# Performance work log

Measured on AMD Instinct MI355X. Metric: run time of the kernel, lower is better.

Reference implementation:

```python
import jax, jax.numpy as jnp
import numpy as np

BATCH = 1
SEQ = 3072
HID = 1024
HEADS = 16
HDIM = HID // HEADS  # 64
NSEQ = 8
SLEN = 380
ROPE_BASE = 10.0


def _boundaries():
    b, start = [], 0
    for _ in range(NSEQ):
        b.append((start, start + SLEN))
        start = start + SLEN + 1  # +1 for SEP token
    return b


def setup_inputs() -> dict:
    key = jax.random.key(0)
    ks = jax.random.split(key, 10)
    bnd = _boundaries()
    L = bnd[-1][1]  # actual_length = 3047
    # block-diagonal mask; SEP tokens attend only to themselves
    mask = np.zeros((L, L), dtype=bool)
    for s, e in bnd:
        mask[s:e, s:e] = True
    for s, e in bnd[:-1]:
        mask[e, e] = True
    # position ids reset at each sequence start
    pos = np.zeros((SEQ,), dtype=np.int32)
    for s, e in bnd:
        pos[s:e] = np.arange(e - s, dtype=np.int32)
    sc = 1.0 / np.sqrt(HID)
    return {
        "x": jax.random.normal(ks[0], (BATCH, SEQ, HID), jnp.float32),
        "wq": jax.random.normal(ks[1], (HID, HID), jnp.float32) * sc,
        "bq": jnp.zeros((HID,), jnp.float32),
        "wk": jax.random.normal(ks[2], (HID, HID), jnp.float32) * sc,
        "bk": jnp.zeros((HID,), jnp.float32),
        "wv": jax.random.normal(ks[3], (HID, HID), jnp.float32) * sc,
        "bv": jnp.zeros((HID,), jnp.float32),
        "wo": jax.random.normal(ks[4], (HID, HID), jnp.float32) * sc,
        "bo": jnp.zeros((HID,), jnp.float32),
        "mask": jnp.asarray(mask),
        "position_ids": jnp.asarray(pos)[None, :],  # [1, SEQ]
    }


def _apply_rope(q, k, pos):
    # q, k: [B, S, H, D]; pos: [B, S]
    half = HDIM // 2
    inv_freq = 1.0 / (ROPE_BASE ** (jnp.arange(0, HDIM, 2, dtype=jnp.float32) / HDIM))
    ang = pos.astype(jnp.float32)[..., None] * inv_freq  # [B, S, half]
    cos = jnp.cos(ang)[:, :, None, :]  # [B, S, 1, half]
    sin = jnp.sin(ang)[:, :, None, :]

    def rot(t):
        t1, t2 = t[..., :half], t[..., half:]
        return jnp.concatenate([t1 * cos - t2 * sin, t1 * sin + t2 * cos], axis=-1)

    return rot(q), rot(k)


def reference(x, wq, bq, wk, bk, wv, bv, wo, bo, mask, position_ids):
    B, S, _ = x.shape
    L = mask.shape[0]  # actual_length (static)
    q = (x @ wq.T + bq).reshape(B, S, HEADS, HDIM)
    k = (x @ wk.T + bk).reshape(B, S, HEADS, HDIM)
    v = (x @ wv.T + bv).reshape(B, S, HEADS, HDIM)
    q, k = _apply_rope(q, k, position_ids)
    # [B, H, S, D], trim to packed length
    q = q.transpose(0, 2, 1, 3)[:, :, :L, :]
    k = k.transpose(0, 2, 1, 3)[:, :, :L, :]
    v = v.transpose(0, 2, 1, 3)[:, :, :L, :]
    scores = jnp.einsum("bhqd,bhkd->bhqk", q, k) / jnp.sqrt(jnp.float32(HDIM))
    scores = jnp.where(mask[None, None], scores, -jnp.inf)
    attn = jax.nn.softmax(scores, axis=-1)
    out = jnp.einsum("bhqk,bhkd->bhqd", attn, v)  # [B, H, L, D]
    out = jnp.pad(out, ((0, 0), (0, 0), (0, S - L), (0, 0)))  # zero padded tail
    out = out.transpose(0, 2, 1, 3).reshape(B, S, HID)
    return out @ wo.T + bo
```

## Files before the change

kernel.cpp:

```cpp
#include <hip/hip_runtime.h>

typedef unsigned short u16;
typedef __attribute__((ext_vector_type(8))) short short8;
typedef __attribute__((ext_vector_type(4))) float f32x4;

#define SEQ 3072
#define HID 1024
#define HEADS 16
#define HDIM 64
#define SEGLEN 380
#define SEGSTR 381
#define NSEG 8
#define LTOT 3047
#define VPAD 384

static __device__ __forceinline__ u16 f2bf(float f) {
  unsigned u = __builtin_bit_cast(unsigned, f);
  u += 0x7fffu + ((u >> 16) & 1u);
  return (u16)(u >> 16);
}
static __device__ __forceinline__ float bf2f(u16 h) {
  unsigned u = ((unsigned)h) << 16;
  return __builtin_bit_cast(float, u);
}

static __device__ __forceinline__ void load_lds16(const void* g, void* l) {
  __builtin_amdgcn_global_load_lds((const __attribute__((address_space(1))) void*)g,
                                   (__attribute__((address_space(3))) void*)l, 16, 0, 0);
}

#define BAR() __builtin_amdgcn_s_barrier()
#define VM(N) asm volatile("s_waitcnt vmcnt(" #N ")" ::: "memory")

__global__ void cvt_all_kernel(const float* __restrict__ x, const float* __restrict__ wq,
                               const float* __restrict__ wk, const float* __restrict__ wv,
                               const float* __restrict__ wo, u16* __restrict__ ws) {
  const int d = blockIdx.x * 256 + threadIdx.x;
  const float* src;
  if (d < 393216) {
    const int tm = d >> 14, rem = d & 16383;
    const int tk = rem >> 9, rem2 = rem & 511;
    const int row = rem2 >> 2, cp = rem2 & 3;
    const int j = cp ^ ((row >> 1) & 3);
    src = x + ((size_t)(tm * 128 + row) * HID + tk * 32 + j * 8);
  } else if (d < 786432) {
    const int dd = d - 393216;
    const int tc = dd >> 14, rem = dd & 16383;
    const int tk = rem >> 9, rem2 = rem & 511;
    const int row = rem2 >> 2, cp = rem2 & 3;
    const int j = cp ^ ((row >> 1) & 3);
    const int which = tc >> 3;
    const float* wsrc = (which == 0) ? wq : (which == 1) ? wk : wv;
    src = wsrc + ((size_t)((tc & 7) * 128 + row) * HID + tk * 32 + j * 8);
  } else {
    const int dd = d - 786432;
    const int tc = dd >> 13, rem = dd & 8191;
    const int tk = rem >> 9, rem2 = rem & 511;
    const int row = rem2 >> 3, cp = rem2 & 7;
    const int j = cp ^ (row & 7);
    src = wo + ((size_t)(tc * 64 + row) * HID + tk * 64 + j * 8);
  }
  float4 a = *reinterpret_cast<const float4*>(src);
  float4 b = *reinterpret_cast<const float4*>(src + 4);
  unsigned long long o0 = (unsigned long long)f2bf(a.x) |
                          ((unsigned long long)f2bf(a.y) << 16) |
                          ((unsigned long long)f2bf(a.z) << 32) |
                          ((unsigned long long)f2bf(a.w) << 48);
  unsigned long long o1 = (unsigned long long)f2bf(b.x) |
                          ((unsigned long long)f2bf(b.y) << 16) |
                          ((unsigned long long)f2bf(b.z) << 32) |
                          ((unsigned long long)f2bf(b.w) << 48);
  unsigned long long* dst = reinterpret_cast<unsigned long long*>(ws + (size_t)d * 8);
  dst[0] = o0;
  dst[1] = o1;
}

static __device__ __forceinline__ void stage_qkv(
    const u16* __restrict__ Ablk, const u16* __restrict__ Bblk,
    u16* As, u16* Bs, int t) {
  const int tid = threadIdx.x;
  const int w = tid >> 6;
  load_lds16(Ablk + (size_t)t * 4096 + tid * 8, As + (w * 64) * 8);
  load_lds16(Bblk + (size_t)t * 4096 + tid * 8, Bs + (w * 64) * 8);
}

static __device__ __forceinline__ void compute_qkv(
    const u16* As, const u16* Bs, int wr, int cb0, int lc, int lh, f32x4 (*acc)[2]) {
  short8 af[4], bfv[2];
#pragma unroll
  for (int m = 0; m < 4; ++m) {
    const int row = wr + m * 16 + lc;
    af[m] = *reinterpret_cast<const short8*>(As + row * 32 + (lh ^ ((row >> 1) & 3)) * 8);
  }
#pragma unroll
  for (int n = 0; n < 2; ++n) {
    const int row = cb0 + n * 32 + lc;
    bfv[n] = *reinterpret_cast<const short8*>(Bs + row * 32 + (lh ^ ((row >> 1) & 3)) * 8);
  }
  __builtin_amdgcn_s_setprio(1);
#pragma unroll
  for (int m = 0; m < 4; ++m)
#pragma unroll
    for (int n = 0; n < 2; ++n)
      acc[m][n] = __builtin_amdgcn_mfma_f32_16x16x32_bf16(af[m], bfv[n], acc[m][n], 0, 0, 0);
  __builtin_amdgcn_s_setprio(0);
}

__global__ __launch_bounds__(512) void qkv_gemm_kernel(
    const u16* __restrict__ xblk, const u16* __restrict__ wblk,
    const float* __restrict__ bq, const float* __restrict__ bk, const float* __restrict__ bv,
    u16* __restrict__ qb, u16* __restrict__ kbuf, u16* __restrict__ vT) {
  __shared__ u16 As[3][128 * 32];
  __shared__ u16 Bs[3][128 * 32];
  const int which = blockIdx.y >> 3;
  const float* bias = (which == 0) ? bq : (which == 1) ? bk : bv;
  const int rowBase = blockIdx.x * 128;
  const int colBase = (blockIdx.y & 7) * 128;
  const u16* Ablk = xblk + (size_t)blockIdx.x * 131072;
  const u16* Bblk = wblk + (size_t)blockIdx.y * 131072;
  const int tid = threadIdx.x;
  const int w = tid >> 6, l = tid & 63, lc = l & 15, lh = l >> 4;
  const int wr = (w >> 2) * 64;
  const int c2 = w & 3;
  const int cb0 = (c2 >> 1) * 64 + (c2 & 1) * 16;

  f32x4 acc[4][2];
  f32x4 z4 = {0.f, 0.f, 0.f, 0.f};
#pragma unroll
  for (int m = 0; m < 4; ++m) { acc[m][0] = z4; acc[m][1] = z4; }

  stage_qkv(Ablk, Bblk, As[0], Bs[0], 0);
  stage_qkv(Ablk, Bblk, As[1], Bs[1], 1);
#pragma unroll 1
  for (int t = 0; t < 30; t += 3) {
    stage_qkv(Ablk, Bblk, As[2], Bs[2], t + 2);
    VM(4); BAR();
    compute_qkv(As[0], Bs[0], wr, cb0, lc, lh, acc);
    BAR();
    stage_qkv(Ablk, Bblk, As[0], Bs[0], t + 3);
    VM(4); BAR();
    compute_qkv(As[1], Bs[1], wr, cb0, lc, lh, acc);
    BAR();
    stage_qkv(Ablk, Bblk, As[1], Bs[1], t + 4);
    VM(4); BAR();
    compute_qkv(As[2], Bs[2], wr, cb0, lc, lh, acc);
    BAR();
  }
  VM(2); BAR();
  compute_qkv(As[0], Bs[0], wr, cb0, lc, lh, acc);
  BAR();
  VM(0); BAR();
  compute_qkv(As[1], Bs[1], wr, cb0, lc, lh, acc);

  const int f = (c2 & 1) * 16 + lc;
  const int col0 = colBase + (c2 >> 1) * 64 + f;
  if (which < 2) {
    u16* outp = which ? kbuf : qb;
    const float bv0 = bias[col0];
    const float bv1 = bias[col0 + 32];
    const float invf = exp2f(-(float)f * 0.10381025296523007f);
#pragma unroll
    for (int m = 0; m < 4; ++m) {
      const int row0 = rowBase + wr + m * 16 + lh * 4;
#pragma unroll
      for (int r = 0; r < 4; ++r) {
        const int row = row0 + r;
        const int rr = row % SEGSTR;
        const float pos = (float)((rr < SEGLEN) ? rr : 0);
        float sn, cs;
        sincosf(pos * invf, &sn, &cs);
        const float t1 = acc[m][0][r] + bv0;
        const float t2 = acc[m][1][r] + bv1;
        const size_t base = (size_t)row * HID + col0;
        outp[base] = f2bf(t1 * cs - t2 * sn);
        outp[base + 32] = f2bf(t1 * sn + t2 * cs);
      }
    }
  } else {
#pragma unroll
    for (int n = 0; n < 2; ++n) {
      const int col = col0 + n * 32;
      const float bvl = bias[col];
#pragma unroll
      for (int m = 0; m < 4; ++m) {
        const int row0 = rowBase + wr + m * 16 + lh * 4;
#pragma unroll
        for (int r = 0; r < 4; ++r) {
          const float v = acc[m][n][r] + bvl;
          const int row = row0 + r;
          const int sg = row / SEGSTR;
          const int j = row - sg * SEGSTR;
          if (sg < NSEG)
            vT[(size_t)col * (NSEG * VPAD) + sg * VPAD + j] = f2bf(v);
        }
      }
    }
  }
}

static __device__ __forceinline__ void stage_out(
    const u16* __restrict__ Ab, const u16* __restrict__ Bb,
    u16* As, u16* Bs, int t) {
  const int tid = threadIdx.x;
  const int w = tid >> 6;
#pragma unroll
  for (int c = 0; c < 2; ++c)
    load_lds16(Ab + (size_t)t * 8192 + (c * 512 + tid) * 8, As + (c * 512 + w * 64) * 8);
  load_lds16(Bb + (size_t)t * 4096 + tid * 8, Bs + (w * 64) * 8);
}

static __device__ __forceinline__ void compute_out(
    const u16* As, const u16* Bs, int wrO, int wcO, int lc, int lh, f32x4 (*acc)[2]) {
  short8 af[2][2], bfv[2][2];
#pragma unroll
  for (int m = 0; m < 2; ++m) {
    const int row = wrO + m * 16 + lc;
#pragma unroll
    for (int ks = 0; ks < 2; ++ks)
      af[m][ks] = *reinterpret_cast<const short8*>(
          As + row * 64 + (((ks * 4 + lh) ^ (row & 7))) * 8);
  }
#pragma unroll
  for (int n = 0; n < 2; ++n) {
    const int row = wcO + n * 16 + lc;
#pragma unroll
    for (int ks = 0; ks < 2; ++ks)
      bfv[n][ks] = *reinterpret_cast<const short8*>(
          Bs + row * 64 + (((ks * 4 + lh) ^ (row & 7))) * 8);
  }
  __builtin_amdgcn_s_setprio(1);
#pragma unroll
  for (int ks = 0; ks < 2; ++ks)
#pragma unroll
    for (int m = 0; m < 2; ++m)
#pragma unroll
      for (int n = 0; n < 2; ++n)
        acc[m][n] = __builtin_amdgcn_mfma_f32_16x16x32_bf16(af[m][ks], bfv[n][ks], acc[m][n], 0, 0, 0);
  __builtin_amdgcn_s_setprio(0);
}

__global__ __launch_bounds__(512) void out_gemm_kernel(
    const u16* __restrict__ aoblk, const u16* __restrict__ woblk,
    const float* __restrict__ bo, float* __restrict__ out) {
  __shared__ u16 As[3][128 * 64];
  __shared__ u16 Bs[3][64 * 64];
  const int bx = blockIdx.x, by = blockIdx.y;
  const int rowBase = bx * 128;
  const int colBase = by * 64;
  const u16* Ab = aoblk + (size_t)bx * 16 * 8192;
  const u16* Bb = woblk + (size_t)by * 16 * 4096;
  const int tid = threadIdx.x;
  const int w = tid >> 6, l = tid & 63, lc = l & 15, lh = l >> 4;
  const int wrO = (w >> 1) * 32, wcO = (w & 1) * 32;
  f32x4 acc[2][2];
  f32x4 z4 = {0.f, 0.f, 0.f, 0.f};
#pragma unroll
  for (int m = 0; m < 2; ++m) { acc[m][0] = z4; acc[m][1] = z4; }

  stage_out(Ab, Bb, As[0], Bs[0], 0);
  stage_out(Ab, Bb, As[1], Bs[1], 1);
#pragma unroll 1
  for (int t = 0; t < 12; t += 3) {
    stage_out(Ab, Bb, As[2], Bs[2], t + 2);
    VM(6); BAR();
    compute_out(As[0], Bs[0], wrO, wcO, lc, lh, acc);
    BAR();
    stage_out(Ab, Bb, As[0], Bs[0], t + 3);
    VM(6); BAR();
    compute_out(As[1], Bs[1], wrO, wcO, lc, lh, acc);
    BAR();
    stage_out(Ab, Bb, As[1], Bs[1], t + 4);
    VM(6); BAR();
    compute_out(As[2], Bs[2], wrO, wcO, lc, lh, acc);
    BAR();
  }
  stage_out(Ab, Bb, As[2], Bs[2], 14);
  VM(6); BAR();
  compute_out(As[0], Bs[0], wrO, wcO, lc, lh, acc);
  BAR();
  stage_out(Ab, Bb, As[0], Bs[0], 15);
  VM(6); BAR();
  compute_out(As[1], Bs[1], wrO, wcO, lc, lh, acc);
  BAR();
  VM(3); BAR();
  compute_out(As[2], Bs[2], wrO, wcO, lc, lh, acc);
  BAR();
  VM(0); BAR();
  compute_out(As[0], Bs[0], wrO, wcO, lc, lh, acc);

#pragma unroll
  for (int n = 0; n < 2; ++n) {
    const int col = colBase + wcO + n * 16 + lc;
    const float bvl = bo[col];
#pragma unroll
    for (int m = 0; m < 2; ++m) {
      const int row0 = rowBase + wrO + m * 16 + lh * 4;
#pragma unroll
      for (int r = 0; r < 4; ++r)
        out[(size_t)(row0 + r) * HID + col] = acc[m][n][r] + bvl;
    }
  }
}

__global__ __launch_bounds__(256) void attn_kernel(
    const u16* __restrict__ qb, const u16* __restrict__ kb,
    const u16* __restrict__ vT, u16* __restrict__ ao) {
  __shared__ u16 Ks[3][32 * 64];
  __shared__ u16 Vs[3][64 * 32];
  __shared__ u16 P_lds[4][16 * 32];
  const int tid = threadIdx.x;
  const int w = tid >> 6, l = tid & 63, lc = l & 15, lh = l >> 4;
  const int W = (blockIdx.x & 7) * 96 + (blockIdx.x >> 3);
  const int qt = W % 6;
  const int seg = (W / 6) & 7;
  const int h = W / 48;
  const int segbase = seg * SEGSTR;
  const int rloc = qt * 64 + w * 16;

  const u16* qrow = qb + (size_t)(segbase + rloc + lc) * HID + h * HDIM + lh * 8;
  const short8 qf0 = *reinterpret_cast<const short8*>(qrow);
  const short8 qf1 = *reinterpret_cast<const short8*>(qrow + 32);

  const size_t vstride = (size_t)NSEG * VPAD;
  const u16* kseg = kb + (size_t)segbase * HID + h * HDIM;
  const u16* vseg = vT + (size_t)h * HDIM * vstride + seg * VPAD;

  const int krow = tid >> 3;
  const int kj = (tid & 7) ^ (krow & 7);
  const int vd = tid >> 2;
  const int vj = (tid & 3) ^ ((vd >> 2) & 3);

  f32x4 z4 = {0.f, 0.f, 0.f, 0.f};
  f32x4 accO[4] = {z4, z4, z4, z4};
  float psum[4] = {0.f, 0.f, 0.f, 0.f};

  u16* pl = &P_lds[w][0];
  int wo0[4], wo1[4];
#pragma unroll
  for (int r = 0; r < 4; ++r) {
    const int prow = lh * 4 + r;
    const int sw = (prow >> 1) & 3;
    wo0[r] = prow * 32 + ((lc >> 3) ^ sw) * 8 + (lc & 7);
    wo1[r] = prow * 32 + ((2 + (lc >> 3)) ^ sw) * 8 + (lc & 7);
  }
  const int prd_off = lc * 32 + (lh ^ ((lc >> 1) & 3)) * 8;

#define STAGE(B, T)                                                                 \
  load_lds16(kseg + (size_t)((T) * 32 + krow) * HID + kj * 8, &Ks[B][0] + w * 512); \
  load_lds16(vseg + (size_t)vd * vstride + (T) * 32 + vj * 8, &Vs[B][0] + w * 512);

#define STEP(B, MASKED)                                                               \
  {                                                                                   \
    const u16* KB = &Ks[B][0];                                                        \
    const u16* VB = &Vs[B][0];                                                        \
    const int ks0 = (lh ^ (lc & 7)) * 8;                                              \
    const int ks1 = ((lh + 4) ^ (lc & 7)) * 8;                                        \
    const short8 k00 = *reinterpret_cast<const short8*>(KB + lc * 64 + ks0);          \
    const short8 k01 = *reinterpret_cast<const short8*>(KB + lc * 64 + ks1);          \
    const short8 k10 = *reinterpret_cast<const short8*>(KB + (16 + lc) * 64 + ks0);   \
    const short8 k11 = *reinterpret_cast<const short8*>(KB + (16 + lc) * 64 + ks1);   \
    f32x4 s0 = z4, s1 = z4;                                                           \
    __builtin_amdgcn_s_setprio(1);                                                    \
    s0 = __builtin_amdgcn_mfma_f32_16x16x32_bf16(qf0, k00, s0, 0, 0, 0);              \
    s0 = __builtin_amdgcn_mfma_f32_16x16x32_bf16(qf1, k01, s0, 0, 0, 0);              \
    s1 = __builtin_amdgcn_mfma_f32_16x16x32_bf16(qf0, k10, s1, 0, 0, 0);              \
    s1 = __builtin_amdgcn_mfma_f32_16x16x32_bf16(qf1, k11, s1, 0, 0, 0);              \
    __builtin_amdgcn_s_setprio(0);                                                    \
    float p0[4], p1[4];                                                               \
    _Pragma("unroll") for (int r = 0; r < 4; ++r) {                                   \
      p0[r] = (!(MASKED) || lc < 28) ? __expf(s0[r] * 0.125f) : 0.f;                  \
      p1[r] = (!(MASKED) || lc < 12) ? __expf(s1[r] * 0.125f) : 0.f;                  \
      psum[r] += p0[r] + p1[r];                                                       \
    }                                                                                 \
    _Pragma("unroll") for (int r = 0; r < 4; ++r) {                                   \
      pl[wo0[r]] = f2bf(p0[r]);                                                       \
      pl[wo1[r]] = f2bf(p1[r]);                                                       \
    }                                                                                 \
    const short8 pf = *reinterpret_cast<const short8*>(pl + prd_off);                 \
    const int vsw = (lh ^ (lc >> 2)) * 8;                                             \
    const short8 v0 = *reinterpret_cast<const short8*>(VB + lc * 32 + vsw);           \
    const short8 v1 = *reinterpret_cast<const short8*>(VB + (16 + lc) * 32 + vsw);    \
    const short8 v2 = *reinterpret_cast<const short8*>(VB + (32 + lc) * 32 + vsw);    \
    const short8 v3 = *reinterpret_cast<const short8*>(VB + (48 + lc) * 32 + vsw);    \
    __builtin_amdgcn_s_setprio(1);                                                    \
    accO[0] = __builtin_amdgcn_mfma_f32_16x16x32_bf16(pf, v0, accO[0], 0, 0, 0);      \
    accO[1] = __builtin_amdgcn_mfma_f32_16x16x32_bf16(pf, v1, accO[1], 0, 0, 0);      \
    accO[2] = __builtin_amdgcn_mfma_f32_16x16x32_bf16(pf, v2, accO[2], 0, 0, 0);      \
    accO[3] = __builtin_amdgcn_mfma_f32_16x16x32_bf16(pf, v3, accO[3], 0, 0, 0);      \
    __builtin_amdgcn_s_setprio(0);                                                    \
  }

  STAGE(0, 0);
  STAGE(1, 1);
#pragma unroll 1
  for (int t = 0; t < 9; t += 3) {
    STAGE(2, t + 2);
    VM(4); BAR();
    STEP(0, false);
    BAR();
    STAGE(0, t + 3);
    VM(4); BAR();
    STEP(1, false);
    BAR();
    STAGE(1, t + 4);
    VM(4); BAR();
    STEP(2, false);
    BAR();
  }
  STAGE(2, 11);
  VM(4); BAR();
  STEP(0, false);
  BAR();
  VM(2); BAR();
  STEP(1, false);
  BAR();
  VM(0); BAR();
  STEP(2, true);
#undef STEP
#undef STAGE

  float inv[4];
#pragma unroll
  for (int r = 0; r < 4; ++r) {
    float s = psum[r];
    s += __shfl_xor(s, 1);
    s += __shfl_xor(s, 2);
    s += __shfl_xor(s, 4);
    s += __shfl_xor(s, 8);
    inv[r] = 1.0f / s;
  }
#pragma unroll
  for (int r = 0; r < 4; ++r) {
    const int lrow = rloc + lh * 4 + r;
    if (lrow < SEGLEN) {
      const int R = segbase + lrow;
      const size_t base = (size_t)((R >> 7) * 16 + h) * 8192 + (size_t)(R & 127) * 64;
      const int sw = R & 7;
#pragma unroll
      for (int n = 0; n < 4; ++n) {
        const int kk = n * 16 + lc;
        ao[base + (((kk >> 3) ^ sw) * 8) + (kk & 7)] = f2bf(accO[n][r] * inv[r]);
      }
    }
  }

  if (qt == 5) {
    if (seg < NSEG - 1) {
      if (tid < HDIM) {
        const int R = segbase + SEGLEN;
        const size_t base = (size_t)((R >> 7) * 16 + h) * 8192 + (size_t)(R & 127) * 64;
        ao[base + (((tid >> 3) ^ (R & 7)) * 8) + (tid & 7)] =
            vT[(size_t)(h * HDIM + tid) * vstride + seg * VPAD + SEGLEN];
      }
    } else {
#pragma unroll
      for (int k = 0; k < 7; ++k) {
        const int idx = k * 256 + tid;
        if (idx < 25 * HDIM) {
          const int rr = idx >> 6, cc = idx & 63;
          const int R = LTOT + rr;
          const size_t base = (size_t)((R >> 7) * 16 + h) * 8192 + (size_t)(R & 127) * 64;
          ao[base + (((cc >> 3) ^ (R & 7)) * 8) + (cc & 7)] = 0;
        }
      }
    }
  }
}

extern "C" void kernel_launch(void* const* d_in, const int* in_sizes, int n_in,
                              void* d_out, int out_size, void* d_ws, size_t ws_size,
                              hipStream_t stream) {
  const float* x  = (const float*)d_in[0];
  const float* wq = (const float*)d_in[1];
  const float* bq = (const float*)d_in[2];
  const float* wk = (const float*)d_in[3];
  const float* bk = (const float*)d_in[4];
  const float* wv = (const float*)d_in[5];
  const float* bv = (const float*)d_in[6];
  const float* wo = (const float*)d_in[7];
  const float* bo = (const float*)d_in[8];
  float* out = (float*)d_out;

  u16* ws = (u16*)d_ws;
  u16* xblk  = ws;
  u16* wblk  = xblk + (size_t)SEQ * HID;
  u16* woblk = wblk + (size_t)3 * HID * HID;
  u16* qb    = woblk + (size_t)HID * HID;
  u16* kbuf  = qb  + (size_t)SEQ * HID;
  u16* vT    = kbuf + (size_t)SEQ * HID;
  u16* aoblk = vT  + (size_t)HID * (NSEG * VPAD);

  cvt_all_kernel<<<3584, 256, 0, stream>>>(x, wq, wk, wv, wo, ws);

  qkv_gemm_kernel<<<dim3(SEQ / 128, 24), 512, 0, stream>>>(
      xblk, wblk, bq, bk, bv, qb, kbuf, vT);

  attn_kernel<<<768, 256, 0, stream>>>(qb, kbuf, vT, aoblk);

  out_gemm_kernel<<<dim3(SEQ / 128, HID / 64), 512, 0, stream>>>(aoblk, woblk, bo, out);

  (void)in_sizes; (void)n_in; (void)out_size; (void)ws_size;
}
```

Baseline: 73.97 us.

## Store K and V in pre-swizzled per-head tile blocks for contiguous attention staging

The QKV GEMM epilogue now writes K and V into per-(head, segment) 32-row tiles of 2048 elements, already in the XOR-swizzled LDS order. The attention kernel can then stage each tile with one fully contiguous 16-byte load per thread instead of strided row gathers. The conversion kernel gets extra blocks that zero the padding slots in the last tile of each segment. The cost is more scattered 2-byte stores in the GEMM epilogue and more complex index math.

```diff
diff --git a/kernel.cpp b/kernel.cpp
--- a/kernel.cpp
+++ b/kernel.cpp
@@ -12,7 +12,6 @@
 #define SEGSTR 381
 #define NSEG 8
 #define LTOT 3047
-#define VPAD 384
 
 static __device__ __forceinline__ u16 f2bf(float f) {
   unsigned u = __builtin_bit_cast(unsigned, f);
@@ -34,7 +33,22 @@
 
 __global__ void cvt_all_kernel(const float* __restrict__ x, const float* __restrict__ wq,
                                const float* __restrict__ wk, const float* __restrict__ wv,
-                               const float* __restrict__ wo, u16* __restrict__ ws) {
+                               const float* __restrict__ wo, u16* __restrict__ ws,
+                               u16* __restrict__ kblk, u16* __restrict__ vblk) {
+  if (blockIdx.x >= 3584) {
+    const int i = (blockIdx.x - 3584) * 256 + threadIdx.x;
+    if (i < 24576) {
+      const int tile = i / 192, r = i % 192;
+      kblk[(size_t)(tile * 12 + 11) * 2048 + 1856 + r] = 0;
+    } else {
+      const int ii = i - 24576;
+      const int tile = ii / 192, j = ii % 192;
+      const int d = j / 3, kk = 29 + j % 3;
+      vblk[(size_t)(tile * 12 + 11) * 2048 + d * 32 +
+           ((3 ^ ((d >> 2) & 3)) * 8) + (kk & 7)] = 0;
+    }
+    return;
+  }
   const int d = blockIdx.x * 256 + threadIdx.x;
   const float* src;
   if (d < 393216) {
@@ -109,7 +123,7 @@
 __global__ __launch_bounds__(512) void qkv_gemm_kernel(
     const u16* __restrict__ xblk, const u16* __restrict__ wblk,
     const float* __restrict__ bq, const float* __restrict__ bk, const float* __restrict__ bv,
-    u16* __restrict__ qb, u16* __restrict__ kbuf, u16* __restrict__ vT) {
+    u16* __restrict__ qb, u16* __restrict__ kblk, u16* __restrict__ vblk) {
   __shared__ u16 As[3][128 * 32];
   __shared__ u16 Bs[3][128 * 32];
   const int which = blockIdx.y >> 3;
@@ -155,10 +169,10 @@
   const int f = (c2 & 1) * 16 + lc;
   const int col0 = colBase + (c2 >> 1) * 64 + f;
   if (which < 2) {
-    u16* outp = which ? kbuf : qb;
     const float bv0 = bias[col0];
     const float bv1 = bias[col0 + 32];
     const float invf = exp2f(-(float)f * 0.10381025296523007f);
+    const int h = col0 >> 6;
 #pragma unroll
     for (int m = 0; m < 4; ++m) {
       const int row0 = rowBase + wr + m * 16 + lh * 4;
@@ -171,9 +185,22 @@
         sincosf(pos * invf, &sn, &cs);
         const float t1 = acc[m][0][r] + bv0;
         const float t2 = acc[m][1][r] + bv1;
-        const size_t base = (size_t)row * HID + col0;
-        outp[base] = f2bf(t1 * cs - t2 * sn);
-        outp[base + 32] = f2bf(t1 * sn + t2 * cs);
+        const u16 e0 = f2bf(t1 * cs - t2 * sn);
+        const u16 e1 = f2bf(t1 * sn + t2 * cs);
+        if (which == 0) {
+          const size_t base = (size_t)row * HID + col0;
+          qb[base] = e0;
+          qb[base + 32] = e1;
+        } else {
+          const int sg = row / SEGSTR;
+          if (sg < NSEG) {
+            const int jj = row - sg * SEGSTR;
+            const int tt = jj >> 5, kr = jj & 31;
+            const size_t tb = (size_t)((h * 8 + sg) * 12 + tt) * 2048 + kr * 64;
+            kblk[tb + (((f >> 3) ^ (kr & 7)) * 8) + (f & 7)] = e0;
+            kblk[tb + ((((f + 32) >> 3) ^ (kr & 7)) * 8) + (f & 7)] = e1;
+          }
+        }
       }
     }
   } else {
@@ -181,17 +208,21 @@
     for (int n = 0; n < 2; ++n) {
       const int col = col0 + n * 32;
       const float bvl = bias[col];
+      const int h = col >> 6, dd = col & 63;
 #pragma unroll
       for (int m = 0; m < 4; ++m) {
         const int row0 = rowBase + wr + m * 16 + lh * 4;
 #pragma unroll
         for (int r = 0; r < 4; ++r) {
-          const float v = acc[m][n][r] + bvl;
           const int row = row0 + r;
           const int sg = row / SEGSTR;
-          const int j = row - sg * SEGSTR;
-          if (sg < NSEG)
-            vT[(size_t)col * (NSEG * VPAD) + sg * VPAD + j] = f2bf(v);
+          if (sg < NSEG) {
+            const int jj = row - sg * SEGSTR;
+            const int tt = jj >> 5, kk = jj & 31;
+            vblk[(size_t)((h * 8 + sg) * 12 + tt) * 2048 + dd * 32 +
+                 (((kk >> 3) ^ ((dd >> 2) & 3)) * 8) + (kk & 7)] =
+                f2bf(acc[m][n][r] + bvl);
+          }
         }
       }
     }
@@ -303,8 +334,8 @@
 }
 
 __global__ __launch_bounds__(256) void attn_kernel(
-    const u16* __restrict__ qb, const u16* __restrict__ kb,
-    const u16* __restrict__ vT, u16* __restrict__ ao) {
+    const u16* __restrict__ qb, const u16* __restrict__ kblk,
+    const u16* __restrict__ vblk, u16* __restrict__ ao) {
   __shared__ u16 Ks[3][32 * 64];
   __shared__ u16 Vs[3][64 * 32];
   __shared__ u16 P_lds[4][16 * 32];
@@ -321,14 +352,8 @@
   const short8 qf0 = *reinterpret_cast<const short8*>(qrow);
   const short8 qf1 = *reinterpret_cast<const short8*>(qrow + 32);
 
-  const size_t vstride = (size_t)NSEG * VPAD;
-  const u16* kseg = kb + (size_t)segbase * HID + h * HDIM;
-  const u16* vseg = vT + (size_t)h * HDIM * vstride + seg * VPAD;
-
-  const int krow = tid >> 3;
-  const int kj = (tid & 7) ^ (krow & 7);
-  const int vd = tid >> 2;
-  const int vj = (tid & 3) ^ ((vd >> 2) & 3);
+  const u16* ktiles = kblk + (size_t)(h * 8 + seg) * 12 * 2048;
+  const u16* vtiles = vblk + (size_t)(h * 8 + seg) * 12 * 2048;
 
   f32x4 z4 = {0.f, 0.f, 0.f, 0.f};
   f32x4 accO[4] = {z4, z4, z4, z4};
@@ -345,9 +370,9 @@
   }
   const int prd_off = lc * 32 + (lh ^ ((lc >> 1) & 3)) * 8;
 
-#define STAGE(B, T)                                                                 \
-  load_lds16(kseg + (size_t)((T) * 32 + krow) * HID + kj * 8, &Ks[B][0] + w * 512); \
-  load_lds16(vseg + (size_t)vd * vstride + (T) * 32 + vj * 8, &Vs[B][0] + w * 512);
+#define STAGE(B, T)                                                     \
+  load_lds16(ktiles + (size_t)(T) * 2048 + tid * 8, &Ks[B][0] + w * 512); \
+  load_lds16(vtiles + (size_t)(T) * 2048 + tid * 8, &Vs[B][0] + w * 512);
 
 #define STEP(B, MASKED)                                                               \
   {                                                                                   \
@@ -447,10 +472,12 @@
   if (qt == 5) {
     if (seg < NSEG - 1) {
       if (tid < HDIM) {
+        const int dd = tid;
+        const u16 sval = vblk[(size_t)((h * 8 + seg) * 12 + 11) * 2048 + dd * 32 +
+                              ((3 ^ ((dd >> 2) & 3)) * 8) + 4];
         const int R = segbase + SEGLEN;
         const size_t base = (size_t)((R >> 7) * 16 + h) * 8192 + (size_t)(R & 127) * 64;
-        ao[base + (((tid >> 3) ^ (R & 7)) * 8) + (tid & 7)] =
-            vT[(size_t)(h * HDIM + tid) * vstride + seg * VPAD + SEGLEN];
+        ao[base + (((dd >> 3) ^ (R & 7)) * 8) + (dd & 7)] = sval;
       }
     } else {
 #pragma unroll
@@ -486,16 +513,16 @@
   u16* wblk  = xblk + (size_t)SEQ * HID;
   u16* woblk = wblk + (size_t)3 * HID * HID;
   u16* qb    = woblk + (size_t)HID * HID;
-  u16* kbuf  = qb  + (size_t)SEQ * HID;
-  u16* vT    = kbuf + (size_t)SEQ * HID;
-  u16* aoblk = vT  + (size_t)HID * (NSEG * VPAD);
-
-  cvt_all_kernel<<<3584, 256, 0, stream>>>(x, wq, wk, wv, wo, ws);
+  u16* kblk  = qb   + (size_t)SEQ * HID;
+  u16* vblk  = kblk + (size_t)16 * 8 * 12 * 2048;
+  u16* aoblk = vblk + (size_t)16 * 8 * 12 * 2048;
+
+  cvt_all_kernel<<<3776, 256, 0, stream>>>(x, wq, wk, wv, wo, ws, kblk, vblk);
 
   qkv_gemm_kernel<<<dim3(SEQ / 128, 24), 512, 0, stream>>>(
-      xblk, wblk, bq, bk, bv, qb, kbuf, vT);
-
-  attn_kernel<<<768, 256, 0, stream>>>(qb, kbuf, vT, aoblk);
+      xblk, wblk, bq, bk, bv, qb, kblk, vblk);
+
+  attn_kernel<<<768, 256, 0, stream>>>(qb, kblk, vblk, aoblk);
 
   out_gemm_kernel<<<dim3(SEQ / 128, HID / 64), 512, 0, stream>>>(aoblk, woblk, bo, out);
 
```

New measurement: 72.56 us. No clear change (-1.9%).
